# Kernel tuning notes

Measured on AMD Instinct MI355X. Metric: run time of the kernel, lower is better.

The kernel has to match this reference:

```python
import jax, jax.numpy as jnp
import numpy as np

N_NODES = 100000


def gcn_conv(x, edge_index, W, b, n):
    # PyG GCNConv: add self-loops, symmetric normalization, then scatter-add.
    src, dst = edge_index[0], edge_index[1]
    loop = jnp.arange(n, dtype=src.dtype)
    src = jnp.concatenate([src, loop])
    dst = jnp.concatenate([dst, loop])
    h = x @ W  # [n, out]
    deg = jnp.zeros((n,), dtype=x.dtype).at[dst].add(1.0)
    dinv = jnp.where(deg > 0, jax.lax.rsqrt(deg), 0.0)
    norm = dinv[src] * dinv[dst]  # [E+n]
    msg = h[src] * norm[:, None]  # gather + scale
    out = jax.ops.segment_sum(msg, dst, num_segments=n)  # scatter-add
    return out + b


def setup_inputs() -> dict:
    key = jax.random.key(0)
    ks = jax.random.split(key, 6)
    n, f, h, c, e = N_NODES, 128, 32, 7, 3200000
    x = jax.random.normal(ks[0], (n, f), dtype=jnp.float32)
    edge_index = jax.random.randint(ks[1], (2, e), 0, n, dtype=jnp.int64)
    W1 = jax.random.normal(ks[2], (f, h), dtype=jnp.float32) * (1.0 / np.sqrt(f))
    b1 = jnp.zeros((h,), dtype=jnp.float32)
    W2 = jax.random.normal(ks[3], (h, c), dtype=jnp.float32) * (1.0 / np.sqrt(h))
    b2 = jnp.zeros((c,), dtype=jnp.float32)
    return {"x": x, "edge_index": edge_index, "W1": W1, "b1": b1, "W2": W2, "b2": b2}


def reference(x, edge_index, W1, b1, W2, b2):
    n = x.shape[0]
    h = jax.nn.relu(gcn_conv(x, edge_index, W1, b1, n))
    # F.dropout(training=False) is identity in eval mode
    out = gcn_conv(h, edge_index, W2, b2, n)
    return jax.nn.log_softmax(out, axis=1)
```

## Files before the change

kernel.cpp:

```cpp
#include <hip/hip_runtime.h>
#include <math.h>


#define F_IN   128
#define F_HID  32
#define F_OUT  7
#define TILE   8192
#define BSH    8
#define BNODES 256
#define HSZ    512
#define PCAP   10240

typedef __attribute__((ext_vector_type(8))) short bf16x8;
typedef __attribute__((ext_vector_type(4))) float f32x4;
typedef __attribute__((ext_vector_type(4))) int   i32x4;

__device__ __forceinline__ float bf2f(unsigned short u) {
    return __uint_as_float(((unsigned int)u) << 16);
}
__device__ __forceinline__ unsigned short f2bf(float f) {
    unsigned int u = __float_as_uint(f);
    u += 0x7FFF + ((u >> 16) & 1);
    return (unsigned short)(u >> 16);
}
__device__ __forceinline__ unsigned int pack2(unsigned short lo, unsigned short hi) {
    return (unsigned int)lo | ((unsigned int)hi << 16);
}
#define NTL(p) __builtin_nontemporal_load(p)

__global__ __launch_bounds__(512)
void k_tileHist(const int* __restrict__ dst, int E, int NB, int* __restrict__ counts) {
    __shared__ int h[HSZ];
    int tile = blockIdx.x, t = threadIdx.x;
    for (int i = t; i < NB; i += 512) h[i] = 0;
    __syncthreads();
    int base = tile * TILE;
    int lim = base + TILE; if (lim > E) lim = E;
    int n4 = (lim - base) >> 2;
    const i32x4* d4 = (const i32x4*)(dst + base);
    for (int i = t; i < n4; i += 512) {
        i32x4 d = NTL(&d4[i]);
        atomicAdd(&h[d[0] >> BSH], 1);
        atomicAdd(&h[d[1] >> BSH], 1);
        atomicAdd(&h[d[2] >> BSH], 1);
        atomicAdd(&h[d[3] >> BSH], 1);
    }
    __syncthreads();
    for (int i = t; i < NB; i += 512) counts[tile * NB + i] = h[i];
}

__global__ void k_scanA(const int* __restrict__ counts, int NSCAN, int NB, int NT,
                        int* __restrict__ bsum) {
    __shared__ int s[1024];
    int t = threadIdx.x;
    int idx = blockIdx.x * 1024 + t;
    int v = 0;
    if (idx < NSCAN) { int b = idx / NT, tt = idx - b * NT; v = counts[tt * NB + b]; }
    s[t] = v;
    __syncthreads();
    for (int off = 512; off > 0; off >>= 1) {
        if (t < off) s[t] += s[t + off];
        __syncthreads();
    }
    if (t == 0) bsum[blockIdx.x] = s[0];
}

__global__ void k_scanB(int* __restrict__ bsum, int nb) {
    __shared__ int s[1024];
    int t = threadIdx.x;
    int v = (t < nb) ? bsum[t] : 0;
    s[t] = v;
    __syncthreads();
    for (int off = 1; off < 1024; off <<= 1) {
        int a = (t >= off) ? s[t - off] : 0;
        __syncthreads();
        s[t] += a;
        __syncthreads();
    }
    if (t < nb) bsum[t] = s[t] - v;
}

__global__ void k_scanC(const int* __restrict__ counts, int NSCAN, int NB, int NT,
                        const int* __restrict__ bsum, int* __restrict__ tileOffset) {
    __shared__ int s[1024];
    int t = threadIdx.x;
    int idx = blockIdx.x * 1024 + t;
    int v = 0;
    if (idx < NSCAN) { int b = idx / NT, tt = idx - b * NT; v = counts[tt * NB + b]; }
    s[t] = v;
    __syncthreads();
    for (int off = 1; off < 1024; off <<= 1) {
        int a = (t >= off) ? s[t - off] : 0;
        __syncthreads();
        s[t] += a;
        __syncthreads();
    }
    if (idx < NSCAN) tileOffset[idx] = bsum[blockIdx.x] + s[t] - v;
}

__global__ __launch_bounds__(512)
void k_tileFill(const int* __restrict__ src, const int* __restrict__ dst,
                int E, int NB, int NT, const int* __restrict__ tileOffset,
                int* __restrict__ pairBuf) {
    __shared__ int lcur[HSZ];
    int bid = blockIdx.x;
    int xcd = bid & 7;
    int idx = bid >> 3;
    int q = NT >> 3, r = NT & 7;
    int tile = (xcd < r ? xcd * (q + 1) : r * (q + 1) + (xcd - r) * q) + idx;
    int t = threadIdx.x;
    for (int i = t; i < NB; i += 512) lcur[i] = tileOffset[i * NT + tile];
    __syncthreads();
    int base = tile * TILE;
    int lim = base + TILE; if (lim > E) lim = E;
    int n4 = (lim - base) >> 2;
    const i32x4* s4 = (const i32x4*)(src + base);
    const i32x4* d4 = (const i32x4*)(dst + base);
    for (int i = t; i < n4; i += 512) {
        i32x4 s = NTL(&s4[i]);
        i32x4 d = NTL(&d4[i]);
        #pragma unroll
        for (int k = 0; k < 4; ++k) {
            int b = d[k] >> BSH;
            int pos = atomicAdd(&lcur[b], 1);
            pairBuf[pos] = ((d[k] & (BNODES - 1)) << 17) | s[k];
        }
    }
}

__global__ __launch_bounds__(512)
void k_bucketCSR(const int* __restrict__ pairBuf, const int* __restrict__ tileOffset,
                 int NT, int NB, int E, int n,
                 int* __restrict__ degi, int* __restrict__ cursor,
                 float* __restrict__ dinv, int* __restrict__ srcSorted) {
    __shared__ int outb[PCAP];
    __shared__ int cntq[BNODES * 4];
    __shared__ int pref[BNODES * 4];
    __shared__ int sred[BNODES];
    int b = blockIdx.x, t = threadIdx.x;
    for (int i = t; i < BNODES * 4; i += 512) cntq[i] = 0;
    __syncthreads();
    int bs = tileOffset[b * NT];
    int be = (b + 1 < NB) ? tileOffset[(b + 1) * NT] : E;
    int sz = be - bs;
    int th1 = n >> 2, th2 = n >> 1, th3 = (n >> 2) + (n >> 1);
    for (int j = bs + t; j < be; j += 512) {
        int p = pairBuf[j];
        int s = p & 0x1FFFF;
        int q = (s >= th1) + (s >= th2) + (s >= th3);
        atomicAdd(&cntq[((p >> 17) << 2) | q], 1);
    }
    __syncthreads();
    int v0 = 0, v1 = 0, v2 = 0, v3 = 0, sum = 0, base = 0;
    if (t < BNODES) {
        base = t << 2;
        v0 = cntq[base]; v1 = cntq[base + 1]; v2 = cntq[base + 2]; v3 = cntq[base + 3];
        sum = v0 + v1 + v2 + v3;
        sred[t] = sum;
    }
    __syncthreads();
    for (int off = 1; off < BNODES; off <<= 1) {
        int a = (t < BNODES && t >= off) ? sred[t - off] : 0;
        __syncthreads();
        if (t < BNODES) sred[t] += a;
        __syncthreads();
    }
    if (t < BNODES) {
        int ex = sred[t] - sum;
        pref[base]     = ex;
        pref[base + 1] = ex + v0;
        pref[base + 2] = ex + v0 + v1;
        pref[base + 3] = ex + v0 + v1 + v2;
        int node = (b << BSH) + t;
        if (node < n) {
            degi[node]   = sum;
            cursor[node] = bs + ex;
            dinv[node]   = rsqrtf((float)sum + 1.0f);
        }
    }
    __syncthreads();
    for (int j = bs + t; j < be; j += 512) {
        int p = pairBuf[j];
        int s = p & 0x1FFFF;
        int q = (s >= th1) + (s >= th2) + (s >= th3);
        int pos = atomicAdd(&pref[((p >> 17) << 2) | q], 1);
        if (pos < PCAP) outb[pos] = s;
        else            srcSorted[bs + pos] = s;
    }
    __syncthreads();
    int lim = sz < PCAP ? sz : PCAP;
    for (int idx = t; idx < lim; idx += 512) srcSorted[bs + idx] = outb[idx];
}

__global__ void k_wT(const float* __restrict__ W1, unsigned short* __restrict__ Wfrag) {
    int t = threadIdx.x;
    for (int i = 0; i < 16; ++i) {
        int idx = t + i * 256;
        int j = idx & 7;
        int l = (idx >> 3) & 63;
        int f = idx >> 9;
        int nt = f >> 2, ks = f & 3;
        int k = ks * 32 + ((l >> 4) << 3) + j;
        int col = nt * 16 + (l & 15);
        Wfrag[idx] = f2bf(W1[k * F_HID + col]);
    }
}

__global__ void k_gemm1(const float* __restrict__ x, const unsigned short* __restrict__ Wfrag,
                        const float* __restrict__ dinv, unsigned short* __restrict__ g1b,
                        int n) {
    int wave = threadIdx.x >> 6;
    int lane = threadIdx.x & 63;
    int row0 = (blockIdx.x * 4 + wave) * 16;
    if (row0 >= n) return;
    bf16x8 bfr[2][4];
    #pragma unroll
    for (int nt = 0; nt < 2; ++nt)
        #pragma unroll
        for (int ks = 0; ks < 4; ++ks)
            bfr[nt][ks] = *(const bf16x8*)&Wfrag[(((nt << 2) + ks) * 64 + lane) << 3];
    int arow = row0 + (lane & 15);
    const float* xr = x + (size_t)arow * F_IN + ((lane >> 4) << 3);
    f32x4 acc0 = {0.f, 0.f, 0.f, 0.f};
    f32x4 acc1 = {0.f, 0.f, 0.f, 0.f};
    #pragma unroll
    for (int ks = 0; ks < 4; ++ks) {
        f32x4 lo = NTL((const f32x4*)(xr + ks * 32));
        f32x4 hi = NTL((const f32x4*)(xr + ks * 32 + 4));
        bf16x8 a;
        a[0] = (short)f2bf(lo[0]); a[1] = (short)f2bf(lo[1]);
        a[2] = (short)f2bf(lo[2]); a[3] = (short)f2bf(lo[3]);
        a[4] = (short)f2bf(hi[0]); a[5] = (short)f2bf(hi[1]);
        a[6] = (short)f2bf(hi[2]); a[7] = (short)f2bf(hi[3]);
        acc0 = __builtin_amdgcn_mfma_f32_16x16x32_bf16(a, bfr[0][ks], acc0, 0, 0, 0);
        acc1 = __builtin_amdgcn_mfma_f32_16x16x32_bf16(a, bfr[1][ks], acc1, 0, 0, 0);
    }
    int col = lane & 15;
    #pragma unroll
    for (int rr = 0; rr < 4; ++rr) {
        int orow = row0 + ((lane >> 4) << 2) + rr;
        float di = dinv[orow];
        g1b[(size_t)orow * F_HID + col]      = f2bf(acc0[rr] * di);
        g1b[(size_t)orow * F_HID + col + 16] = f2bf(acc1[rr] * di);
    }
}

__global__ void k_gather1l2(const ushort4* __restrict__ g1v, const int* __restrict__ srcSorted,
                            const int* __restrict__ cursor, const int* __restrict__ degi,
                            const float* __restrict__ dinv, const float* __restrict__ b1,
                            const float* __restrict__ W2, unsigned int* __restrict__ g2b,
                            int n) {
    int t = threadIdx.x;
    int c = t & 7;
    int node = blockIdx.x * 32 + (t >> 3);
    if (node >= n) return;
    int start = cursor[node];
    int end = start + degi[node];
    ushort4 sv = g1v[node * 8 + c];
    float ax = bf2f(sv.x), ay = bf2f(sv.y), az = bf2f(sv.z), aw = bf2f(sv.w);
    float bx = 0.f, by = 0.f, bz = 0.f, bw = 0.f;
    float cx = 0.f, cy = 0.f, cz = 0.f, cw = 0.f;
    float dx = 0.f, dy = 0.f, dz = 0.f, dw = 0.f;
    int j = start;
    for (; j + 4 <= end; j += 4) {
        int s0 = srcSorted[j];
        int s1 = srcSorted[j + 1];
        int s2 = srcSorted[j + 2];
        int s3 = srcSorted[j + 3];
        ushort4 v0 = g1v[s0 * 8 + c];
        ushort4 v1 = g1v[s1 * 8 + c];
        ushort4 v2 = g1v[s2 * 8 + c];
        ushort4 v3 = g1v[s3 * 8 + c];
        ax += bf2f(v0.x); ay += bf2f(v0.y); az += bf2f(v0.z); aw += bf2f(v0.w);
        bx += bf2f(v1.x); by += bf2f(v1.y); bz += bf2f(v1.z); bw += bf2f(v1.w);
        cx += bf2f(v2.x); cy += bf2f(v2.y); cz += bf2f(v2.z); cw += bf2f(v2.w);
        dx += bf2f(v3.x); dy += bf2f(v3.y); dz += bf2f(v3.z); dw += bf2f(v3.w);
    }
    for (; j < end; ++j) {
        ushort4 v0 = g1v[srcSorted[j] * 8 + c];
        ax += bf2f(v0.x); ay += bf2f(v0.y); az += bf2f(v0.z); aw += bf2f(v0.w);
    }
    float accx = (ax + bx) + (cx + dx);
    float accy = (ay + by) + (cy + dy);
    float accz = (az + bz) + (cz + dz);
    float accw = (aw + bw) + (cw + dw);
    float di = dinv[node];
    float4 b4 = ((const float4*)b1)[c];
    float hx = fmaxf(di * accx + b4.x, 0.f);
    float hy = fmaxf(di * accy + b4.y, 0.f);
    float hz = fmaxf(di * accz + b4.z, 0.f);
    float hw = fmaxf(di * accw + b4.w, 0.f);
    float p[F_OUT];
    #pragma unroll
    for (int k = 0; k < F_OUT; ++k) {
        p[k] = hx * W2[(4 * c + 0) * F_OUT + k]
             + hy * W2[(4 * c + 1) * F_OUT + k]
             + hz * W2[(4 * c + 2) * F_OUT + k]
             + hw * W2[(4 * c + 3) * F_OUT + k];
    }
    #pragma unroll
    for (int m = 1; m < 8; m <<= 1) {
        #pragma unroll
        for (int k = 0; k < F_OUT; ++k) p[k] += __shfl_xor(p[k], m, 64);
    }
    if (c == 0) {
        uint4 q;
        q.x = pack2(f2bf(di * p[0]), f2bf(di * p[1]));
        q.y = pack2(f2bf(di * p[2]), f2bf(di * p[3]));
        q.z = pack2(f2bf(di * p[4]), f2bf(di * p[5]));
        q.w = pack2(f2bf(di * p[6]), 0);
        *(uint4*)&g2b[node * 4] = q;
    }
}

__global__ void k_gather2final(const unsigned int* __restrict__ g2u,
                               const int* __restrict__ srcSorted,
                               const int* __restrict__ cursor, const int* __restrict__ degi,
                               const float* __restrict__ dinv, const float* __restrict__ b2,
                               float* __restrict__ out, int n) {
    int t = threadIdx.x;
    int c2 = t & 3;
    int node = blockIdx.x * 64 + (t >> 2);
    if (node >= n) return;
    int start = cursor[node];
    int end = start + degi[node];
    unsigned int su = g2u[node * 4 + c2];
    float al = bf2f((unsigned short)su),        ah = bf2f((unsigned short)(su >> 16));
    float bl = 0.f, bh = 0.f, cl = 0.f, ch = 0.f, dl = 0.f, dh = 0.f;
    int j = start;
    for (; j + 4 <= end; j += 4) {
        int s0 = srcSorted[j];
        int s1 = srcSorted[j + 1];
        int s2 = srcSorted[j + 2];
        int s3 = srcSorted[j + 3];
        unsigned int u0 = g2u[s0 * 4 + c2];
        unsigned int u1 = g2u[s1 * 4 + c2];
        unsigned int u2 = g2u[s2 * 4 + c2];
        unsigned int u3 = g2u[s3 * 4 + c2];
        al += bf2f((unsigned short)u0); ah += bf2f((unsigned short)(u0 >> 16));
        bl += bf2f((unsigned short)u1); bh += bf2f((unsigned short)(u1 >> 16));
        cl += bf2f((unsigned short)u2); ch += bf2f((unsigned short)(u2 >> 16));
        dl += bf2f((unsigned short)u3); dh += bf2f((unsigned short)(u3 >> 16));
    }
    for (; j < end; ++j) {
        unsigned int u0 = g2u[srcSorted[j] * 4 + c2];
        al += bf2f((unsigned short)u0); ah += bf2f((unsigned short)(u0 >> 16));
    }
    float accl = (al + bl) + (cl + dl);
    float acch = (ah + bh) + (ch + dh);
    float di = dinv[node];
    float vl = di * accl + b2[2 * c2];
    float vh = (c2 < 3) ? (di * acch + b2[2 * c2 + 1]) : -1e30f;
    float m = fmaxf(vl, vh);
    #pragma unroll
    for (int msk = 1; msk < 4; msk <<= 1) m = fmaxf(m, __shfl_xor(m, msk, 64));
    float ssum = __expf(vl - m) + ((c2 < 3) ? __expf(vh - m) : 0.f);
    #pragma unroll
    for (int msk = 1; msk < 4; msk <<= 1) ssum += __shfl_xor(ssum, msk, 64);
    float ls = __logf(ssum) + m;
    __builtin_nontemporal_store(vl - ls, &out[node * F_OUT + 2 * c2]);
    if (c2 < 3) __builtin_nontemporal_store(vh - ls, &out[node * F_OUT + 2 * c2 + 1]);
}

extern "C" void kernel_launch(void* const* d_in, const int* in_sizes, int n_in,
                              void* d_out, int out_size, void* d_ws, size_t ws_size,
                              hipStream_t stream) {
    const float* x  = (const float*)d_in[0];
    const int*   ei = (const int*)d_in[1];
    const float* W1 = (const float*)d_in[2];
    const float* b1 = (const float*)d_in[3];
    const float* W2 = (const float*)d_in[4];
    const float* b2 = (const float*)d_in[5];
    float* out = (float*)d_out;

    int n = in_sizes[0] / F_IN;
    int E = in_sizes[1] / 2;
    const int* src = ei;
    const int* dst = ei + E;
    int NB = (n + BNODES - 1) >> BSH;
    int NT = (E + TILE - 1) / TILE;
    int NSCAN = NB * NT;
    int nsb = (NSCAN + 1023) / 1024;

    int*            degi       = (int*)d_ws;
    int*            cursor     = degi + n;
    float*          dinv       = (float*)(cursor + n);
    int*            srcSorted  = (int*)(dinv + n);
    int*            pairBuf    = srcSorted + E;
    unsigned short* g1b        = (unsigned short*)pairBuf;
    unsigned short* g2b        = (unsigned short*)(pairBuf + E);
    int*            counts     = (int*)(g2b + (size_t)n * 8);
    int*            tileOffset = counts + NSCAN;
    int*            bsum       = tileOffset + NSCAN;
    unsigned short* Wfrag      = (unsigned short*)(bsum + ((nsb + 3) & ~3));

    k_wT<<<1, 256, 0, stream>>>(W1, Wfrag);
    k_tileHist<<<NT, 512, 0, stream>>>(dst, E, NB, counts);
    k_scanA<<<nsb, 1024, 0, stream>>>(counts, NSCAN, NB, NT, bsum);
    k_scanB<<<1, 1024, 0, stream>>>(bsum, nsb);
    k_scanC<<<nsb, 1024, 0, stream>>>(counts, NSCAN, NB, NT, bsum, tileOffset);
    k_tileFill<<<NT, 512, 0, stream>>>(src, dst, E, NB, NT, tileOffset, pairBuf);
    k_bucketCSR<<<NB, 512, 0, stream>>>(pairBuf, tileOffset, NT, NB, E, n,
                                        degi, cursor, dinv, srcSorted);
    k_gemm1<<<(n + 63) / 64, 256, 0, stream>>>(x, Wfrag, dinv, g1b, n);
    k_gather1l2<<<(n + 31) / 32, 256, 0, stream>>>((const ushort4*)g1b, srcSorted, cursor, degi,
                                                   dinv, b1, W2, (unsigned int*)g2b, n);
    k_gather2final<<<(n + 63) / 64, 256, 0, stream>>>((const unsigned int*)g2b, srcSorted, cursor,
                                                      degi, dinv, b2, out, n);
}
```

Baseline: 143.0 us.

## Widen gather loads to 16B per lane and fold W1 packing into histogram

The first-layer gather now has 4 lanes per node each loading a 16-byte uint4 (8 bf16) instead of 8 lanes loading 8 bytes, halving the shuffle-reduction depth. The second-layer gather now uses one thread per node that loads a whole 16-byte row and does log-softmax in registers, with no cross-lane shuffles. The W1 fragment packing kernel is merged into block 0 of the tile histogram kernel to save one launch. The trade-off is more registers per thread and fewer threads per node, which lowers memory-level parallelism when node degrees vary.

```diff
diff --git a/kernel.cpp b/kernel.cpp
--- a/kernel.cpp
+++ b/kernel.cpp
@@ -28,10 +28,29 @@
 }
 #define NTL(p) __builtin_nontemporal_load(p)
 
+__device__ __forceinline__ void acc8(float* a, uint4 v) {
+    a[0] += bf2f((unsigned short)v.x); a[1] += bf2f((unsigned short)(v.x >> 16));
+    a[2] += bf2f((unsigned short)v.y); a[3] += bf2f((unsigned short)(v.y >> 16));
+    a[4] += bf2f((unsigned short)v.z); a[5] += bf2f((unsigned short)(v.z >> 16));
+    a[6] += bf2f((unsigned short)v.w); a[7] += bf2f((unsigned short)(v.w >> 16));
+}
+
 __global__ __launch_bounds__(512)
-void k_tileHist(const int* __restrict__ dst, int E, int NB, int* __restrict__ counts) {
+void k_tileHist(const int* __restrict__ dst, int E, int NB, int* __restrict__ counts,
+                const float* __restrict__ W1, unsigned short* __restrict__ Wfrag) {
     __shared__ int h[HSZ];
     int tile = blockIdx.x, t = threadIdx.x;
+    if (tile == 0) {
+        for (int idx = t; idx < 4096; idx += 512) {
+            int j = idx & 7;
+            int l = (idx >> 3) & 63;
+            int f = idx >> 9;
+            int nt = f >> 2, ks = f & 3;
+            int k = ks * 32 + ((l >> 4) << 3) + j;
+            int col = nt * 16 + (l & 15);
+            Wfrag[idx] = f2bf(W1[k * F_HID + col]);
+        }
+    }
     for (int i = t; i < NB; i += 512) h[i] = 0;
     __syncthreads();
     int base = tile * TILE;
@@ -192,20 +211,6 @@
     for (int idx = t; idx < lim; idx += 512) srcSorted[bs + idx] = outb[idx];
 }
 
-__global__ void k_wT(const float* __restrict__ W1, unsigned short* __restrict__ Wfrag) {
-    int t = threadIdx.x;
-    for (int i = 0; i < 16; ++i) {
-        int idx = t + i * 256;
-        int j = idx & 7;
-        int l = (idx >> 3) & 63;
-        int f = idx >> 9;
-        int nt = f >> 2, ks = f & 3;
-        int k = ks * 32 + ((l >> 4) << 3) + j;
-        int col = nt * 16 + (l & 15);
-        Wfrag[idx] = f2bf(W1[k * F_HID + col]);
-    }
-}
-
 __global__ void k_gemm1(const float* __restrict__ x, const unsigned short* __restrict__ Wfrag,
                         const float* __restrict__ dinv, unsigned short* __restrict__ g1b,
                         int n) {
@@ -245,61 +250,52 @@
     }
 }
 
-__global__ void k_gather1l2(const ushort4* __restrict__ g1v, const int* __restrict__ srcSorted,
+__global__ void k_gather1l2(const uint4* __restrict__ g1q, const int* __restrict__ srcSorted,
                             const int* __restrict__ cursor, const int* __restrict__ degi,
                             const float* __restrict__ dinv, const float* __restrict__ b1,
-                            const float* __restrict__ W2, unsigned int* __restrict__ g2b,
-                            int n) {
-    int t = threadIdx.x;
-    int c = t & 7;
-    int node = blockIdx.x * 32 + (t >> 3);
+                            const float* __restrict__ W2, uint4* __restrict__ g2q, int n) {
+    int t = threadIdx.x;
+    int c = t & 3;
+    int node = blockIdx.x * 64 + (t >> 2);
     if (node >= n) return;
     int start = cursor[node];
     int end = start + degi[node];
-    ushort4 sv = g1v[node * 8 + c];
-    float ax = bf2f(sv.x), ay = bf2f(sv.y), az = bf2f(sv.z), aw = bf2f(sv.w);
-    float bx = 0.f, by = 0.f, bz = 0.f, bw = 0.f;
-    float cx = 0.f, cy = 0.f, cz = 0.f, cw = 0.f;
-    float dx = 0.f, dy = 0.f, dz = 0.f, dw = 0.f;
+    float a[8], b[8], cc[8], d[8];
+    uint4 sv = g1q[node * 4 + c];
+    #pragma unroll
+    for (int f = 0; f < 8; ++f) { a[f] = 0.f; b[f] = 0.f; cc[f] = 0.f; d[f] = 0.f; }
+    acc8(a, sv);
     int j = start;
     for (; j + 4 <= end; j += 4) {
         int s0 = srcSorted[j];
         int s1 = srcSorted[j + 1];
         int s2 = srcSorted[j + 2];
         int s3 = srcSorted[j + 3];
-        ushort4 v0 = g1v[s0 * 8 + c];
-        ushort4 v1 = g1v[s1 * 8 + c];
-        ushort4 v2 = g1v[s2 * 8 + c];
-        ushort4 v3 = g1v[s3 * 8 + c];
-        ax += bf2f(v0.x); ay += bf2f(v0.y); az += bf2f(v0.z); aw += bf2f(v0.w);
-        bx += bf2f(v1.x); by += bf2f(v1.y); bz += bf2f(v1.z); bw += bf2f(v1.w);
-        cx += bf2f(v2.x); cy += bf2f(v2.y); cz += bf2f(v2.z); cw += bf2f(v2.w);
-        dx += bf2f(v3.x); dy += bf2f(v3.y); dz += bf2f(v3.z); dw += bf2f(v3.w);
-    }
-    for (; j < end; ++j) {
-        ushort4 v0 = g1v[srcSorted[j] * 8 + c];
-        ax += bf2f(v0.x); ay += bf2f(v0.y); az += bf2f(v0.z); aw += bf2f(v0.w);
-    }
-    float accx = (ax + bx) + (cx + dx);
-    float accy = (ay + by) + (cy + dy);
-    float accz = (az + bz) + (cz + dz);
-    float accw = (aw + bw) + (cw + dw);
+        uint4 v0 = g1q[s0 * 4 + c];
+        uint4 v1 = g1q[s1 * 4 + c];
+        uint4 v2 = g1q[s2 * 4 + c];
+        uint4 v3 = g1q[s3 * 4 + c];
+        acc8(a, v0); acc8(b, v1); acc8(cc, v2); acc8(d, v3);
+    }
+    for (; j < end; ++j) acc8(a, g1q[srcSorted[j] * 4 + c]);
     float di = dinv[node];
-    float4 b4 = ((const float4*)b1)[c];
-    float hx = fmaxf(di * accx + b4.x, 0.f);
-    float hy = fmaxf(di * accy + b4.y, 0.f);
-    float hz = fmaxf(di * accz + b4.z, 0.f);
-    float hw = fmaxf(di * accw + b4.w, 0.f);
+    float h[8];
+    #pragma unroll
+    for (int f = 0; f < 8; ++f) {
+        float acc = (a[f] + b[f]) + (cc[f] + d[f]);
+        float v = di * acc + b1[8 * c + f];
+        h[f] = v > 0.f ? v : 0.f;
+    }
     float p[F_OUT];
     #pragma unroll
     for (int k = 0; k < F_OUT; ++k) {
-        p[k] = hx * W2[(4 * c + 0) * F_OUT + k]
-             + hy * W2[(4 * c + 1) * F_OUT + k]
-             + hz * W2[(4 * c + 2) * F_OUT + k]
-             + hw * W2[(4 * c + 3) * F_OUT + k];
-    }
-    #pragma unroll
-    for (int m = 1; m < 8; m <<= 1) {
+        float s = 0.f;
+        #pragma unroll
+        for (int f = 0; f < 8; ++f) s += h[f] * W2[(8 * c + f) * F_OUT + k];
+        p[k] = s;
+    }
+    #pragma unroll
+    for (int m = 1; m < 4; m <<= 1) {
         #pragma unroll
         for (int k = 0; k < F_OUT; ++k) p[k] += __shfl_xor(p[k], m, 64);
     }
@@ -309,57 +305,51 @@
         q.y = pack2(f2bf(di * p[2]), f2bf(di * p[3]));
         q.z = pack2(f2bf(di * p[4]), f2bf(di * p[5]));
         q.w = pack2(f2bf(di * p[6]), 0);
-        *(uint4*)&g2b[node * 4] = q;
-    }
-}
-
-__global__ void k_gather2final(const unsigned int* __restrict__ g2u,
+        g2q[node] = q;
+    }
+}
+
+__global__ void k_gather2final(const uint4* __restrict__ g2q,
                                const int* __restrict__ srcSorted,
                                const int* __restrict__ cursor, const int* __restrict__ degi,
                                const float* __restrict__ dinv, const float* __restrict__ b2,
                                float* __restrict__ out, int n) {
-    int t = threadIdx.x;
-    int c2 = t & 3;
-    int node = blockIdx.x * 64 + (t >> 2);
+    int node = blockIdx.x * 256 + threadIdx.x;
     if (node >= n) return;
     int start = cursor[node];
     int end = start + degi[node];
-    unsigned int su = g2u[node * 4 + c2];
-    float al = bf2f((unsigned short)su),        ah = bf2f((unsigned short)(su >> 16));
-    float bl = 0.f, bh = 0.f, cl = 0.f, ch = 0.f, dl = 0.f, dh = 0.f;
+    float A[8], B[8];
+    #pragma unroll
+    for (int f = 0; f < 8; ++f) { A[f] = 0.f; B[f] = 0.f; }
+    acc8(A, g2q[node]);
     int j = start;
     for (; j + 4 <= end; j += 4) {
         int s0 = srcSorted[j];
         int s1 = srcSorted[j + 1];
         int s2 = srcSorted[j + 2];
         int s3 = srcSorted[j + 3];
-        unsigned int u0 = g2u[s0 * 4 + c2];
-        unsigned int u1 = g2u[s1 * 4 + c2];
-        unsigned int u2 = g2u[s2 * 4 + c2];
-        unsigned int u3 = g2u[s3 * 4 + c2];
-        al += bf2f((unsigned short)u0); ah += bf2f((unsigned short)(u0 >> 16));
-        bl += bf2f((unsigned short)u1); bh += bf2f((unsigned short)(u1 >> 16));
-        cl += bf2f((unsigned short)u2); ch += bf2f((unsigned short)(u2 >> 16));
-        dl += bf2f((unsigned short)u3); dh += bf2f((unsigned short)(u3 >> 16));
-    }
-    for (; j < end; ++j) {
-        unsigned int u0 = g2u[srcSorted[j] * 4 + c2];
-        al += bf2f((unsigned short)u0); ah += bf2f((unsigned short)(u0 >> 16));
-    }
-    float accl = (al + bl) + (cl + dl);
-    float acch = (ah + bh) + (ch + dh);
+        uint4 r0 = g2q[s0];
+        uint4 r1 = g2q[s1];
+        uint4 r2 = g2q[s2];
+        uint4 r3 = g2q[s3];
+        acc8(A, r0); acc8(B, r1); acc8(A, r2); acc8(B, r3);
+    }
+    for (; j < end; ++j) acc8(A, g2q[srcSorted[j]]);
     float di = dinv[node];
-    float vl = di * accl + b2[2 * c2];
-    float vh = (c2 < 3) ? (di * acch + b2[2 * c2 + 1]) : -1e30f;
-    float m = fmaxf(vl, vh);
-    #pragma unroll
-    for (int msk = 1; msk < 4; msk <<= 1) m = fmaxf(m, __shfl_xor(m, msk, 64));
-    float ssum = __expf(vl - m) + ((c2 < 3) ? __expf(vh - m) : 0.f);
-    #pragma unroll
-    for (int msk = 1; msk < 4; msk <<= 1) ssum += __shfl_xor(ssum, msk, 64);
+    float v[F_OUT];
+    float m = -1e30f;
+    #pragma unroll
+    for (int k = 0; k < F_OUT; ++k) {
+        v[k] = di * (A[k] + B[k]) + b2[k];
+        m = fmaxf(m, v[k]);
+    }
+    float ssum = 0.f;
+    #pragma unroll
+    for (int k = 0; k < F_OUT; ++k) ssum += __expf(v[k] - m);
     float ls = __logf(ssum) + m;
-    __builtin_nontemporal_store(vl - ls, &out[node * F_OUT + 2 * c2]);
-    if (c2 < 3) __builtin_nontemporal_store(vh - ls, &out[node * F_OUT + 2 * c2 + 1]);
+    #pragma unroll
+    for (int k = 0; k < F_OUT; ++k)
+        __builtin_nontemporal_store(v[k] - ls, &out[node * F_OUT + k]);
 }
 
 extern "C" void kernel_launch(void* const* d_in, const int* in_sizes, int n_in,
@@ -394,8 +384,7 @@
     int*            bsum       = tileOffset + NSCAN;
     unsigned short* Wfrag      = (unsigned short*)(bsum + ((nsb + 3) & ~3));
 
-    k_wT<<<1, 256, 0, stream>>>(W1, Wfrag);
-    k_tileHist<<<NT, 512, 0, stream>>>(dst, E, NB, counts);
+    k_tileHist<<<NT, 512, 0, stream>>>(dst, E, NB, counts, W1, Wfrag);
     k_scanA<<<nsb, 1024, 0, stream>>>(counts, NSCAN, NB, NT, bsum);
     k_scanB<<<1, 1024, 0, stream>>>(bsum, nsb);
     k_scanC<<<nsb, 1024, 0, stream>>>(counts, NSCAN, NB, NT, bsum, tileOffset);
@@ -403,8 +392,8 @@
     k_bucketCSR<<<NB, 512, 0, stream>>>(pairBuf, tileOffset, NT, NB, E, n,
                                         degi, cursor, dinv, srcSorted);
     k_gemm1<<<(n + 63) / 64, 256, 0, stream>>>(x, Wfrag, dinv, g1b, n);
-    k_gather1l2<<<(n + 31) / 32, 256, 0, stream>>>((const ushort4*)g1b, srcSorted, cursor, degi,
-                                                   dinv, b1, W2, (unsigned int*)g2b, n);
-    k_gather2final<<<(n + 63) / 64, 256, 0, stream>>>((const unsigned int*)g2b, srcSorted, cursor,
-                                                      degi, dinv, b2, out, n);
-}
+    k_gather1l2<<<(n + 63) / 64, 256, 0, stream>>>((const uint4*)g1b, srcSorted, cursor, degi,
+                                                   dinv, b1, W2, (uint4*)g2b, n);
+    k_gather2final<<<(n + 255) / 256, 256, 0, stream>>>((const uint4*)g2b, srcSorted, cursor,
+                                                        degi, dinv, b2, out, n);
+}
```

After: 144.4 us. No clear change (+0.9%).
